# Kernel optimization log

Hardware: AMD Instinct MI355X
Metric: run time of the kernel (lower is better)

Reference implementation:

```python
import jax, jax.numpy as jnp
import numpy as np

HIDDEN = 2560
NUM_HEADS = 80
HEAD_DIM = 64
STATE = 128
N_GROUPS = 1
CONV_K = 4
CHUNK = 256
INTER = 2 * HIDDEN                       # 5120 = NUM_HEADS * HEAD_DIM
CONV_DIM = INTER + 2 * N_GROUPS * STATE  # 5376
PROJ = INTER + CONV_DIM + NUM_HEADS      # 10576
EPS = 1e-5
DT_MIN, DT_MAX = 0.0, 100.0


def segment_sum(x):
    # x: (..., T) -> (..., T, T); out[i, j] = sum_{j < k <= i} x[k], -inf above diag
    T = x.shape[-1]
    xe = jnp.broadcast_to(x[..., :, None], x.shape + (T,))  # [i, j] = x[i]
    mask_lo = jnp.tril(jnp.ones((T, T), dtype=bool), -1)
    seg = jnp.cumsum(jnp.where(mask_lo, xe, 0.0), axis=-2)
    mask = jnp.tril(jnp.ones((T, T), dtype=bool), 0)
    return jnp.where(mask, seg, -jnp.inf)


def setup_inputs() -> dict:
    key = jax.random.key(0)
    k0, k1, k2, k3 = jax.random.split(key, 4)
    x = jax.random.normal(k0, (2, 2048, HIDDEN), jnp.float32)
    in_proj_w = jax.random.normal(k1, (PROJ, HIDDEN), jnp.float32) * (HIDDEN ** -0.5)
    conv1d_w = jax.random.normal(k2, (CONV_DIM, CONV_K), jnp.float32) * (CONV_K ** -0.5)
    conv1d_b = jnp.zeros((CONV_DIM,), jnp.float32)
    A_log = jnp.log(jnp.arange(1, NUM_HEADS + 1, dtype=jnp.float32))
    D = jnp.ones((NUM_HEADS,), jnp.float32)
    dt_bias = jnp.ones((NUM_HEADS,), jnp.float32)
    norm_weight = jnp.ones((INTER,), jnp.float32)
    out_proj_w = jax.random.normal(k3, (HIDDEN, INTER), jnp.float32) * (INTER ** -0.5)
    return dict(input_states=x, in_proj_w=in_proj_w, conv1d_w=conv1d_w,
                conv1d_b=conv1d_b, A_log=A_log, D=D, dt_bias=dt_bias,
                norm_weight=norm_weight, out_proj_w=out_proj_w)


def _mamba2_forward(input_states, in_proj_w, conv1d_w, conv1d_b, A_log, D,
                    dt_bias, norm_weight, out_proj_w):
    b, s, _ = input_states.shape
    proj = input_states @ in_proj_w.T                       # (b, s, PROJ)
    gate, hs, dt = jnp.split(proj, [INTER, INTER + CONV_DIM], axis=-1)

    # causal depthwise conv1d + SiLU
    xT = jnp.transpose(hs, (0, 2, 1))                       # (b, conv_dim, s)
    xT = jnp.pad(xT, ((0, 0), (0, 0), (CONV_K - 1, 0)))
    conv = jax.lax.conv_general_dilated(
        xT, conv1d_w[:, None, :], (1,), 'VALID',
        feature_group_count=CONV_DIM, dimension_numbers=('NCH', 'OIH', 'NCH'))
    hs = jax.nn.silu(jnp.transpose(conv + conv1d_b[None, :, None], (0, 2, 1)))

    hs, B, C = jnp.split(hs, [INTER, INTER + N_GROUPS * STATE], axis=-1)
    A = -jnp.exp(A_log)                                     # (h,)
    dt = jnp.clip(jax.nn.softplus(dt + dt_bias), DT_MIN, DT_MAX)  # (b, s, h)

    X = hs.reshape(b, s, NUM_HEADS, HEAD_DIM)
    rep = NUM_HEADS // N_GROUPS
    B = jnp.repeat(B.reshape(b, s, N_GROUPS, STATE), rep, axis=2)
    C = jnp.repeat(C.reshape(b, s, N_GROUPS, STATE), rep, axis=2)

    pad = (-s) % CHUNK
    D_res = D[None, None, :, None] * jnp.pad(X, ((0, 0), (0, pad), (0, 0), (0, 0)))
    Xd = X * dt[..., None]                                  # discretized input
    dA = A[None, None, :] * dt                              # (b, s, h)

    def chunk(t):
        t = jnp.pad(t, [(0, 0), (0, pad)] + [(0, 0)] * (t.ndim - 2))
        return t.reshape(t.shape[0], -1, CHUNK, *t.shape[2:])

    Xc, Bc, Cc = chunk(Xd), chunk(B), chunk(C)              # (b, c, l, h, ...)
    Ac = jnp.transpose(chunk(dA), (0, 3, 1, 2))             # (b, h, c, l)
    A_cum = jnp.cumsum(Ac, axis=-1)

    # 1. intra-chunk (diagonal block) outputs
    L = jnp.exp(segment_sum(Ac))                            # (b, h, c, l, l)
    G = jnp.einsum('bclhn,bcshn->bhcls', Cc, Bc)
    Y_diag = jnp.einsum('bhcls,bcshp->bclhp', G * L, Xc)

    # 2. per-chunk final states
    decay_states = jnp.exp(A_cum[..., -1:] - A_cum)         # (b, h, c, l)
    states = jnp.einsum('bclhn,bhcl,bclhp->bchpn', Bc, decay_states, Xc)

    # 3. inter-chunk recurrence
    A_last = A_cum[..., -1]                                 # (b, h, c)
    decay_chunk = jnp.exp(segment_sum(jnp.pad(A_last, ((0, 0), (0, 0), (1, 0)))))
    states = jnp.concatenate([jnp.zeros_like(states[:, :1]), states], axis=1)
    new_states = jnp.einsum('bhzc,bchpn->bzhpn', decay_chunk, states)
    states = new_states[:, :-1]                             # (b, c, h, p, n)

    # 4. state -> output conversion
    Y_off = jnp.einsum('bclhn,bchpn,bhcl->bclhp', Cc, states, jnp.exp(A_cum))

    y = (Y_diag + Y_off).reshape(b, -1, NUM_HEADS, HEAD_DIM) + D_res
    y = y[:, :s].reshape(b, s, INTER)

    # gated RMSNorm
    y = y * jax.nn.silu(gate)
    var = jnp.mean(y * y, axis=-1, keepdims=True)
    y = y * jax.lax.rsqrt(var + EPS) * norm_weight
    return y @ out_proj_w.T


def reference(input_states, in_proj_w, conv1d_w, conv1d_b, A_log, D, dt_bias,
              norm_weight, out_proj_w):
    return _mamba2_forward(input_states, in_proj_w, conv1d_w, conv1d_b, A_log,
                           D, dt_bias, norm_weight, out_proj_w)
```

## Files before the change

kernel.cpp:

```cpp
#include <hip/hip_runtime.h>
#include <hip/hip_bf16.h>
#include <math.h>

#define HIDDEN   2560
#define NUM_HEADS 80
#define HEAD_DIM 64
#define STATE    128
#define CONV_K   4
#define CHUNK    256
#define INTER    (2*HIDDEN)
#define CONV_DIM (INTER + 2*STATE)
#define PROJ     (INTER + CONV_DIM + NUM_HEADS)
#define PROJ_PAD 10240
#define NBC      336
#define NBCP     384
#define EPS      1e-5f

#define BATCH 2
#define SEQ   2048
#define TOK   (BATCH*SEQ)
#define NC    (SEQ/CHUNK)
#define KSPL2 8
#define KCH2  (HIDDEN/KSPL2)

typedef __attribute__((ext_vector_type(8))) short bf16x8;
typedef __attribute__((ext_vector_type(4))) float f32x4;

#define MFMA16(a,b,c) __builtin_amdgcn_mfma_f32_16x16x32_bf16((a),(b),(c),0,0,0)

__device__ __forceinline__ unsigned short f2bf(float f){
    union{float f;unsigned u;}v; v.f=f;
    unsigned r = v.u + 0x7fffu + ((v.u>>16)&1u);
    return (unsigned short)(r>>16);
}
__device__ __forceinline__ float bf2f(unsigned short s){
    union{unsigned u;float f;}v; v.u = ((unsigned)s)<<16; return v.f;
}
__device__ __forceinline__ void unpack8(uint4 u, float* e){
    e[0]=bf2f((unsigned short)(u.x&0xffff)); e[1]=bf2f((unsigned short)(u.x>>16));
    e[2]=bf2f((unsigned short)(u.y&0xffff)); e[3]=bf2f((unsigned short)(u.y>>16));
    e[4]=bf2f((unsigned short)(u.z&0xffff)); e[5]=bf2f((unsigned short)(u.z>>16));
    e[6]=bf2f((unsigned short)(u.w&0xffff)); e[7]=bf2f((unsigned short)(u.w>>16));
}

__device__ __forceinline__ void gld16(const void* g, void* l){
    __builtin_amdgcn_global_load_lds((const __attribute__((address_space(1))) void*)g,
                                     (__attribute__((address_space(3))) void*)l, 16, 0, 0);
}

template<bool BF16OUT>
__global__ __launch_bounds__(256) void gemm_bf16(const unsigned short* __restrict__ A, int lda,
                                                 const unsigned short* __restrict__ B, int ldb,
                                                 void* __restrict__ Cv, int ldc, int K) {
    __shared__ unsigned short As[128][64];
    __shared__ unsigned short Bs[128][64];
    int tid = threadIdx.x;
    int lane = tid & 63, wid = tid >> 6;
    int wr = wid >> 1, wc = wid & 1;

    int bm, bn;
    if ((gridDim.y & 7) == 0) {
        int bid   = blockIdx.y * gridDim.x + blockIdx.x;
        int xcd   = bid & 7;
        int local = bid >> 3;
        int mrows = gridDim.y >> 3;
        bm = (xcd * mrows + (local % mrows)) * 128;
        bn = (local / mrows) * 128;
    } else {
        bm = blockIdx.y * 128;
        bn = blockIdx.x * 128;
    }

    f32x4 acc[4][4];
    #pragma unroll
    for (int i=0;i<4;i++)
        #pragma unroll
        for (int j=0;j<4;j++) acc[i][j] = (f32x4){0.f,0.f,0.f,0.f};

    int srow_off = lane >> 3;
    int sslot    = lane & 7;

    for (int k0 = 0; k0 < K; k0 += 64) {
        #pragma unroll
        for (int q=0;q<4;q++){
            int brow = (wid*4+q)*8;
            int row  = brow + srow_off;
            int sl   = sslot ^ (row & 7);
            gld16(A + (size_t)(bm + row)*lda + k0 + sl*8, &As[brow][0]);
            gld16(B + (size_t)(bn + row)*ldb + k0 + sl*8, &Bs[brow][0]);
        }
        __syncthreads();
        #pragma unroll
        for (int kk=0; kk<64; kk+=32){
            bf16x8 a[4], b[4];
            #pragma unroll
            for (int i=0;i<4;i++){
                int row = wr*64 + i*16 + (lane&15);
                int slot = ((kk>>3) + (lane>>4)) ^ (row & 7);
                a[i] = *(const bf16x8*)&As[row][slot*8];
            }
            #pragma unroll
            for (int j=0;j<4;j++){
                int row = wc*64 + j*16 + (lane&15);
                int slot = ((kk>>3) + (lane>>4)) ^ (row & 7);
                b[j] = *(const bf16x8*)&Bs[row][slot*8];
            }
            #pragma unroll
            for (int i=0;i<4;i++)
                #pragma unroll
                for (int j=0;j<4;j++)
                    acc[i][j] = MFMA16(a[i], b[j], acc[i][j]);
        }
        __syncthreads();
    }
    #pragma unroll
    for (int i=0;i<4;i++){
        int row0 = bm + wr*64 + i*16 + (lane>>4)*4;
        #pragma unroll
        for (int j=0;j<4;j++){
            int col = bn + wc*64 + j*16 + (lane&15);
            #pragma unroll
            for (int r=0;r<4;r++){
                if (BF16OUT)
                    ((unsigned short*)Cv)[(size_t)(row0+r)*ldc + col] = f2bf(acc[i][j][r]);
                else
                    ((float*)Cv)[(size_t)(row0+r)*ldc + col] = acc[i][j][r];
            }
        }
    }
}

__global__ __launch_bounds__(256) void bc_splitk_mfma(const unsigned short* __restrict__ xhi,
                                                      const unsigned short* __restrict__ xlo,
                                                      const unsigned short* __restrict__ whi,
                                                      const unsigned short* __restrict__ wlo,
                                                      float* __restrict__ Cpart) {
    __shared__ unsigned short As[128][64];
    __shared__ unsigned short Bs[128][64];
    int tid = threadIdx.x;
    int lane = tid & 63, wid = tid >> 6;
    int wr = wid >> 1, wc = wid & 1;
    int bn = blockIdx.x * 128, bm = blockIdx.y * 128, z = blockIdx.z;

    f32x4 acc[4][4];
    #pragma unroll
    for (int i=0;i<4;i++)
        #pragma unroll
        for (int j=0;j<4;j++) acc[i][j] = (f32x4){0.f,0.f,0.f,0.f};

    int srow_off = lane >> 3;
    int sslot    = lane & 7;

    for (int term = 0; term < 3; ++term){
        const unsigned short* A = (term==2) ? xlo : xhi;
        const unsigned short* B = (term==0) ? wlo : whi;
        for (int k0 = z*KCH2; k0 < z*KCH2 + KCH2; k0 += 64) {
            #pragma unroll
            for (int q=0;q<4;q++){
                int brow = (wid*4+q)*8;
                int row  = brow + srow_off;
                int sl   = sslot ^ (row & 7);
                gld16(A + (size_t)(bm + row)*HIDDEN + k0 + sl*8, &As[brow][0]);
                gld16(B + (size_t)(bn + row)*HIDDEN + k0 + sl*8, &Bs[brow][0]);
            }
            __syncthreads();
            #pragma unroll
            for (int kk=0; kk<64; kk+=32){
                bf16x8 a[4], b[4];
                #pragma unroll
                for (int i=0;i<4;i++){
                    int row = wr*64 + i*16 + (lane&15);
                    int slot = ((kk>>3) + (lane>>4)) ^ (row & 7);
                    a[i] = *(const bf16x8*)&As[row][slot*8];
                }
                #pragma unroll
                for (int j=0;j<4;j++){
                    int row = wc*64 + j*16 + (lane&15);
                    int slot = ((kk>>3) + (lane>>4)) ^ (row & 7);
                    b[j] = *(const bf16x8*)&Bs[row][slot*8];
                }
                #pragma unroll
                for (int i=0;i<4;i++)
                    #pragma unroll
                    for (int j=0;j<4;j++)
                        acc[i][j] = MFMA16(a[i], b[j], acc[i][j]);
            }
            __syncthreads();
        }
    }
    float* Cz = Cpart + (size_t)z*TOK*NBCP;
    #pragma unroll
    for (int i=0;i<4;i++){
        int row0 = bm + wr*64 + i*16 + (lane>>4)*4;
        #pragma unroll
        for (int j=0;j<4;j++){
            int col = bn + wc*64 + j*16 + (lane&15);
            #pragma unroll
            for (int r=0;r<4;r++)
                Cz[(size_t)(row0+r)*NBCP + col] = acc[i][j][r];
        }
    }
}

__global__ __launch_bounds__(256) void reduce_bc2(const float* __restrict__ part,
                                                  const float* __restrict__ dt_bias,
                                                  float* __restrict__ outBC,
                                                  float* __restrict__ dtbuf) {
    size_t i4 = (size_t)blockIdx.x*256 + threadIdx.x;
    if (i4 >= (size_t)TOK*NBCP/4) return;
    size_t i = i4*4;
    float4 s = *(const float4*)(part + i);
    #pragma unroll
    for (int z=1; z<KSPL2; z++){
        float4 v = *(const float4*)(part + (size_t)z*TOK*NBCP + i);
        s.x += v.x; s.y += v.y; s.z += v.z; s.w += v.w;
    }
    int col = (int)(i % NBCP);
    int t   = (int)(i / NBCP);
    if (col < 256) {
        *(float4*)(outBC + (size_t)t*NBC + col) = s;
    } else if (col < NBC) {
        int h = col - 256;
        float e[4] = {s.x, s.y, s.z, s.w};
        #pragma unroll
        for (int u=0;u<4;u++){
            float xv = e[u] + dt_bias[h+u];
            float sp = (xv > 20.f) ? xv : log1pf(expf(xv));
            e[u] = fminf(fmaxf(sp, 0.f), 100.f);
        }
        float4 o; o.x=e[0]; o.y=e[1]; o.z=e[2]; o.w=e[3];
        *(float4*)(dtbuf + (size_t)t*NUM_HEADS + h) = o;
    }
}

#define N4A ((size_t)TOK*HIDDEN/4)
#define N4B ((size_t)PROJ_PAD*HIDDEN/4)
#define N4C ((size_t)NBCP*HIDDEN/4)
__global__ __launch_bounds__(256) void prep_kernel(const float* __restrict__ x,
                                                   const float* __restrict__ in_w,
                                                   unsigned short* __restrict__ xhi,
                                                   unsigned short* __restrict__ xlo,
                                                   unsigned short* __restrict__ w1b,
                                                   unsigned short* __restrict__ wbc_hi,
                                                   unsigned short* __restrict__ wbc_lo) {
    size_t gid = (size_t)blockIdx.x*256 + threadIdx.x;
    if (gid < N4A) {
        size_t i = gid*4;
        float4 v = *(const float4*)(x + i);
        float e[4] = {v.x, v.y, v.z, v.w};
        ushort4 h, l;
        unsigned short* hp = (unsigned short*)&h;
        unsigned short* lp = (unsigned short*)&l;
        #pragma unroll
        for (int u=0;u<4;u++){
            unsigned short hv = f2bf(e[u]);
            hp[u] = hv;
            lp[u] = f2bf(e[u] - bf2f(hv));
        }
        *(ushort4*)(xhi + i) = h;
        *(ushort4*)(xlo + i) = l;
    } else if (gid < N4A + N4B) {
        size_t i = (gid - N4A)*4;
        float4 v = *(const float4*)(in_w + i);
        ushort4 o;
        o.x=f2bf(v.x); o.y=f2bf(v.y); o.z=f2bf(v.z); o.w=f2bf(v.w);
        *(ushort4*)(w1b + i) = o;
    } else {
        size_t j = gid - N4A - N4B;
        size_t i = j*4;
        int row = (int)(i / HIDDEN);
        int kk  = (int)(i % HIDDEN);
        ushort4 h, l;
        h.x=h.y=h.z=h.w=0; l.x=l.y=l.z=l.w=0;
        if (row < NBC){
            float4 v = *(const float4*)(in_w + (size_t)(2*INTER + row)*HIDDEN + kk);
            float e[4] = {v.x, v.y, v.z, v.w};
            unsigned short* hp = (unsigned short*)&h;
            unsigned short* lp = (unsigned short*)&l;
            #pragma unroll
            for (int u=0;u<4;u++){
                unsigned short hv = f2bf(e[u]);
                hp[u] = hv;
                lp[u] = f2bf(e[u] - bf2f(hv));
            }
        }
        *(ushort4*)(wbc_hi + i) = h;
        *(ushort4*)(wbc_lo + i) = l;
    }
}

__global__ __launch_bounds__(256) void cvt_bf16(const float* __restrict__ in,
                                                unsigned short* __restrict__ out, size_t n4){
    size_t i4 = (size_t)blockIdx.x*256 + threadIdx.x;
    if (i4 >= n4) return;
    size_t i = i4*4;
    float4 v = *(const float4*)(in+i);
    ushort4 o; o.x=f2bf(v.x); o.y=f2bf(v.y); o.z=f2bf(v.z); o.w=f2bf(v.w);
    *(ushort4*)(out+i) = o;
}

__global__ __launch_bounds__(256) void conv_fused(const unsigned short* __restrict__ projb,
                                                  const float* __restrict__ projBC,
                                                  const float* __restrict__ cw,
                                                  const float* __restrict__ cb,
                                                  unsigned short* __restrict__ XT,
                                                  float* __restrict__ xBC_BC,
                                                  unsigned short* __restrict__ BT,
                                                  unsigned short* __restrict__ Cb) {
    __shared__ unsigned short raw[68][66];
    int bid = blockIdx.x;
    int tid = threadIdx.x;
    if (bid < (TOK/64)*(INTER/64)) {
        int bx = bid & 63, by = bid >> 6;
        int t0 = bx * 64, d0 = by * 64;
        int b  = t0 / SEQ;
        int s0 = t0 % SEQ;
        for (int f = tid; f < 67*8; f += 256){
            int r = f >> 3, g = f & 7;
            int sp = s0 - 3 + r;
            uint4 v;
            if (sp >= 0) v = *(const uint4*)(projb + ((size_t)(b*SEQ+sp))*PROJ_PAD + INTER + d0 + g*8);
            else { v.x=0u; v.y=0u; v.z=0u; v.w=0u; }
            unsigned int* dst = (unsigned int*)&raw[r][g*8];
            dst[0]=v.x; dst[1]=v.y; dst[2]=v.z; dst[3]=v.w;
        }
        __syncthreads();
        int t = tid & 63, dg = tid >> 6;
        #pragma unroll
        for (int dd = 0; dd < 16; dd++){
            int d = dg*16 + dd;
            float acc = cb[d0+d];
            #pragma unroll
            for (int j=0;j<CONV_K;j++)
                acc += cw[(d0+d)*CONV_K+j] * bf2f(raw[t+j][d]);
            float val = acc/(1.f+expf(-acc));
            XT[((size_t)(b*INTER + d0 + d))*SEQ + s0 + t] = f2bf(val);
        }
    } else {
        int idx = (bid - (TOK/64)*(INTER/64))*256 + tid;
        if (idx >= TOK*256) return;
        int d = idx & 255;
        int t = idx >> 8;
        int b = t / SEQ, sl = t % SEQ;
        int dc = INTER + d;
        float acc = cb[dc];
        #pragma unroll
        for (int j=0;j<CONV_K;j++){
            int sp = sl - (CONV_K-1) + j;
            if (sp >= 0)
                acc += cw[dc*CONV_K+j] * projBC[((size_t)(b*SEQ+sp))*NBC + d];
        }
        float val = acc / (1.f + expf(-acc));
        xBC_BC[(size_t)t*256 + d] = val;
        if (d < 128)
            BT[((size_t)(b*128 + d))*SEQ + sl] = f2bf(val);
        else
            Cb[(size_t)t*128 + (d-128)] = f2bf(val);
    }
}

__global__ __launch_bounds__(256) void cumsum_kernel(const float* __restrict__ dtbuf,
                                                     const float* __restrict__ A_log,
                                                     float* __restrict__ A_cum) {
    int c = blockIdx.x, h = blockIdx.y, b = blockIdx.z;
    int l = threadIdx.x;
    float A = -expf(A_log[h]);
    float v = A * dtbuf[(size_t)(b*SEQ + c*CHUNK + l)*NUM_HEADS + h];
    __shared__ float buf[CHUNK];
    buf[l] = v;
    __syncthreads();
    for (int off=1; off<CHUNK; off<<=1){
        float t = (l>=off) ? buf[l-off] : 0.f;
        __syncthreads();
        buf[l] += t;
        __syncthreads();
    }
    A_cum[((size_t)b*NUM_HEADS + h)*SEQ + c*CHUNK + l] = buf[l];
}

__global__ __launch_bounds__(256) void g_kernel(const float* __restrict__ xBC_BC,
                                                unsigned short* __restrict__ G) {
    int p = blockIdx.x, c = blockIdx.y, b = blockIdx.z;
    int lt = 0, a0 = 0;
    while (a0 + lt + 1 <= p) { a0 += lt + 1; lt++; }
    int st = p - a0;
    int l0 = lt*64, s0 = st*64;
    __shared__ float Cs[64][68];
    __shared__ float Bs[64][68];
    int tid = threadIdx.x, ty = tid >> 4, tx = tid & 15;
    float acc[4][4];
    #pragma unroll
    for (int i=0;i<4;i++)
        #pragma unroll
        for (int j=0;j<4;j++) acc[i][j]=0.f;

    size_t rowC = ((size_t)(b*SEQ + c*CHUNK + l0))*256 + 128;
    size_t rowB = ((size_t)(b*SEQ + c*CHUNK + s0))*256;
    for (int kc=0; kc<2; kc++){
        #pragma unroll
        for (int it=0; it<4; it++){
            int f = tid + it*256;
            int r = f >> 4, c4 = f & 15;
            float4 cv = *(const float4*)(xBC_BC + rowC + (size_t)r*256 + kc*64 + c4*4);
            float4 bv = *(const float4*)(xBC_BC + rowB + (size_t)r*256 + kc*64 + c4*4);
            *(float4*)&Cs[r][c4*4] = cv;
            *(float4*)&Bs[r][c4*4] = bv;
        }
        __syncthreads();
        #pragma unroll 8
        for (int k=0;k<64;k++){
            float a[4], bb[4];
            #pragma unroll
            for (int i=0;i<4;i++) a[i] = Cs[ty*4+i][k];
            #pragma unroll
            for (int j=0;j<4;j++) bb[j] = Bs[tx*4+j][k];
            #pragma unroll
            for (int i=0;i<4;i++)
                #pragma unroll
                for (int j=0;j<4;j++) acc[i][j] += a[i]*bb[j];
        }
        __syncthreads();
    }
    size_t Gb = ((size_t)(b*NC + c)) << 16;
    #pragma unroll
    for (int i=0;i<4;i++){
        ushort4 g4;
        g4.x = f2bf(acc[i][0]); g4.y = f2bf(acc[i][1]);
        g4.z = f2bf(acc[i][2]); g4.w = f2bf(acc[i][3]);
        *(ushort4*)(G + Gb + (size_t)(l0 + ty*4 + i)*256 + s0 + tx*4) = g4;
    }
}

__global__ __launch_bounds__(256) void states_mfma(const unsigned short* __restrict__ XT,
                                                   const unsigned short* __restrict__ BT,
                                                   const float* __restrict__ dtbuf,
                                                   const float* __restrict__ A_cum,
                                                   unsigned short* __restrict__ statesT) {
    int c = blockIdx.x, h = blockIdx.y, b = blockIdx.z;
    __shared__ unsigned short Asx[64][64];
    __shared__ unsigned short Bs[128][64];
    __shared__ float wl[CHUNK];
    int tid = threadIdx.x, lane = tid & 63, wid = tid >> 6;
    {
        const float* ac = A_cum + ((size_t)(b*NUM_HEADS+h))*SEQ + c*CHUNK;
        float Alast = ac[CHUNK-1];
        wl[tid] = expf(Alast - ac[tid]) * dtbuf[((size_t)(b*SEQ + c*CHUNK + tid))*NUM_HEADS + h];
    }
    __syncthreads();
    f32x4 acc[4][2];
    #pragma unroll
    for (int i=0;i<4;i++)
        #pragma unroll
        for (int j=0;j<2;j++) acc[i][j] = (f32x4){0.f,0.f,0.f,0.f};

    for (int kc = 0; kc < 4; kc++){
        int lbase = kc*64;
        #pragma unroll
        for (int q=0;q<4;q++){
            int brow = (wid*4+q)*8;
            int row  = brow + (lane>>3);
            int sl   = (lane&7) ^ (row & 7);
            gld16(BT + ((size_t)(b*128 + row))*SEQ + c*CHUNK + lbase + sl*8, &Bs[brow][0]);
        }
        #pragma unroll
        for (int it=0; it<2; it++){
            int f = tid + it*256;
            int r = f >> 3, g = f & 7;
            uint4 v = *(const uint4*)(XT + ((size_t)(b*INTER + h*HEAD_DIM + r))*SEQ + c*CHUNK + lbase + g*8);
            float e[8]; unpack8(v, e);
            unsigned short o[8];
            #pragma unroll
            for (int u=0;u<8;u++) o[u] = f2bf(e[u] * wl[lbase + g*8 + u]);
            int slot = g ^ (r & 7);
            *(ushort4*)&Asx[r][slot*8]   = *(ushort4*)&o[0];
            *(ushort4*)&Asx[r][slot*8+4] = *(ushort4*)&o[4];
        }
        __syncthreads();
        #pragma unroll
        for (int kk=0; kk<64; kk+=32){
            bf16x8 a[4], bb[2];
            #pragma unroll
            for (int i=0;i<4;i++){
                int row = i*16 + (lane&15);
                int slot = ((kk>>3)+(lane>>4)) ^ (row&7);
                a[i] = *(const bf16x8*)&Asx[row][slot*8];
            }
            #pragma unroll
            for (int j=0;j<2;j++){
                int row = wid*32 + j*16 + (lane&15);
                int slot = ((kk>>3)+(lane>>4)) ^ (row&7);
                bb[j] = *(const bf16x8*)&Bs[row][slot*8];
            }
            #pragma unroll
            for (int i=0;i<4;i++)
                #pragma unroll
                for (int j=0;j<2;j++)
                    acc[i][j] = MFMA16(a[i], bb[j], acc[i][j]);
        }
        __syncthreads();
    }
    size_t sb = ((size_t)((b*NC + c)*NUM_HEADS + h))*(HEAD_DIM*STATE);
    #pragma unroll
    for (int i=0;i<4;i++){
        #pragma unroll
        for (int j=0;j<2;j++){
            int n = wid*32 + j*16 + (lane&15);
            int p0 = i*16 + (lane>>4)*4;
            #pragma unroll
            for (int r=0;r<4;r++)
                statesT[sb + (size_t)(p0+r)*128 + n] = f2bf(acc[i][j][r]);
        }
    }
}

__global__ __launch_bounds__(256) void recur_kernel(const float* __restrict__ A_cum,
                                                    unsigned short* __restrict__ states) {
    int h = blockIdx.x, b = blockIdx.y;
    int tid = threadIdx.x;
    float Srun[32];
    #pragma unroll
    for (int i=0;i<32;i++) Srun[i]=0.f;
    const float* acum = A_cum + ((size_t)b*NUM_HEADS + h)*SEQ;
    for (int c=0;c<NC;c++){
        float alast = acum[c*CHUNK + CHUNK-1];
        float dec = expf(alast);
        size_t base = ((size_t)((b*NC + c)*NUM_HEADS + h))*(HEAD_DIM*STATE);
        #pragma unroll
        for (int i=0;i<32;i++){
            size_t idx = base + (size_t)tid + (size_t)i*256;
            float raw = bf2f(states[idx]);
            states[idx] = f2bf(Srun[i]);
            Srun[i] = Srun[i]*dec + raw;
        }
    }
}

__global__ __launch_bounds__(256) void yscan_mfma(const unsigned short* __restrict__ G,
                                                  const unsigned short* __restrict__ Cb,
                                                  const unsigned short* __restrict__ XT,
                                                  const float* __restrict__ dtbuf,
                                                  const float* __restrict__ A_cum,
                                                  const unsigned short* __restrict__ statesT,
                                                  const float* __restrict__ Dvec,
                                                  unsigned short* __restrict__ projb) {
    int xb = blockIdx.x;
    int c = xb >> 2, lt = xb & 3;
    int h = blockIdx.y, b = blockIdx.z;
    int l0 = lt*64;
    __shared__ __align__(16) char pool[32768];
    unsigned short (*Cs)[128] = (unsigned short(*)[128])pool;
    unsigned short (*St)[128] = (unsigned short(*)[128])(pool + 16384);
    unsigned short (*Gw)[64]  = (unsigned short(*)[64])pool;
    unsigned short (*Xs)[64]  = (unsigned short(*)[64])(pool + 8192);
    float (*Ot)[68]           = (float(*)[68])pool;
    __shared__ float ac[CHUNK], dts[CHUNK];
    int tid = threadIdx.x, lane = tid & 63, wid = tid >> 6;
    ac[tid]  = A_cum[((size_t)(b*NUM_HEADS + h))*SEQ + c*CHUNK + tid];
    dts[tid] = dtbuf[((size_t)(b*SEQ + c*CHUNK + tid))*NUM_HEADS + h];

    size_t stb = ((size_t)((b*NC + c)*NUM_HEADS + h))*(HEAD_DIM*STATE);
    #pragma unroll
    for (int q=0;q<4;q++){
        int brow = (wid*4+q)*4;
        int row  = brow + (lane>>4);
        int sl   = (lane&15) ^ (row & 7);
        gld16(Cb + ((size_t)(b*SEQ + c*CHUNK + l0 + row))*128 + sl*8, &Cs[brow][0]);
        gld16(statesT + stb + (size_t)row*128 + sl*8, &St[brow][0]);
    }
    __syncthreads();

    f32x4 acc1[4];
    #pragma unroll
    for (int j=0;j<4;j++) acc1[j] = (f32x4){0.f,0.f,0.f,0.f};
    #pragma unroll
    for (int kk=0; kk<128; kk+=32){
        int arow = wid*16 + (lane&15);
        int aslot = ((kk>>3)+(lane>>4)) ^ (arow&7);
        bf16x8 a = *(const bf16x8*)&Cs[arow][aslot*8];
        #pragma unroll
        for (int j=0;j<4;j++){
            int brow = j*16 + (lane&15);
            int bslot = ((kk>>3)+(lane>>4)) ^ (brow&7);
            bf16x8 bb = *(const bf16x8*)&St[brow][bslot*8];
            acc1[j] = MFMA16(a, bb, acc1[j]);
        }
    }
    float el[4];
    #pragma unroll
    for (int r=0;r<4;r++) el[r] = expf(ac[l0 + wid*16 + (lane>>4)*4 + r]);
    float master[4][4];
    #pragma unroll
    for (int j=0;j<4;j++)
        #pragma unroll
        for (int r=0;r<4;r++) master[j][r] = acc1[j][r]*el[r];
    __syncthreads();

    size_t Gb = ((size_t)(b*NC + c)) << 16;
    f32x4 acc2[4];
    #pragma unroll
    for (int j=0;j<4;j++) acc2[j] = (f32x4){0.f,0.f,0.f,0.f};
    for (int st=0; st<=lt; st++){
        int s0 = st*64;
        #pragma unroll
        for (int it=0; it<2; it++){
            int f = tid + it*256;
            int r = f >> 3, g = f & 7;
            uint4 v = *(const uint4*)(G + Gb + (size_t)(l0 + r)*256 + s0 + g*8);
            float e[8]; unpack8(v, e);
            float acl = ac[l0 + r];
            unsigned short o[8];
            #pragma unroll
            for (int u=0;u<8;u++){
                int s = s0 + g*8 + u;
                float w = (s <= l0 + r) ? expf(acl - ac[s])*dts[s] : 0.f;
                o[u] = f2bf(e[u]*w);
            }
            int slot = g ^ (r&7);
            *(ushort4*)&Gw[r][slot*8]   = *(ushort4*)&o[0];
            *(ushort4*)&Gw[r][slot*8+4] = *(ushort4*)&o[4];
        }
        #pragma unroll
        for (int q=0;q<2;q++){
            int brow = (wid*2+q)*8;
            int row  = brow + (lane>>3);
            int sl   = (lane&7) ^ (row&7);
            gld16(XT + ((size_t)(b*INTER + h*HEAD_DIM + row))*SEQ + c*CHUNK + s0 + sl*8,
                  &Xs[brow][0]);
        }
        __syncthreads();
        #pragma unroll
        for (int kk=0; kk<64; kk+=32){
            int arow = wid*16 + (lane&15);
            int aslot = ((kk>>3)+(lane>>4)) ^ (arow&7);
            bf16x8 a = *(const bf16x8*)&Gw[arow][aslot*8];
            #pragma unroll
            for (int j=0;j<4;j++){
                int brow = j*16 + (lane&15);
                int bslot = ((kk>>3)+(lane>>4)) ^ (brow&7);
                bf16x8 bb = *(const bf16x8*)&Xs[brow][bslot*8];
                acc2[j] = MFMA16(a, bb, acc2[j]);
            }
        }
        if (st < lt) __syncthreads();
    }

    float Dh = Dvec[h];
    #pragma unroll
    for (int j=0;j<4;j++){
        int p = j*16 + (lane&15);
        #pragma unroll
        for (int r=0;r<4;r++){
            int sl_ = wid*16 + (lane>>4)*4 + r;
            int slot = (sl_>>3) ^ (p&7);
            float xv = bf2f(Xs[p][slot*8 + (sl_&7)]);
            master[j][r] += acc2[j][r] + Dh*xv;
        }
    }
    __syncthreads();

    #pragma unroll
    for (int j=0;j<4;j++){
        int p = j*16 + (lane&15);
        #pragma unroll
        for (int r=0;r<4;r++)
            Ot[wid*16 + (lane>>4)*4 + r][p] = master[j][r];
    }
    __syncthreads();
    #pragma unroll
    for (int it=0; it<4; it++){
        int f = tid + it*256;
        int r = f >> 4, c4 = f & 15;
        ushort4 o;
        o.x = f2bf(Ot[r][c4*4+0]); o.y = f2bf(Ot[r][c4*4+1]);
        o.z = f2bf(Ot[r][c4*4+2]); o.w = f2bf(Ot[r][c4*4+3]);
        *(ushort4*)(projb + ((size_t)(b*SEQ + c*CHUNK + l0 + r))*PROJ_PAD + INTER + h*HEAD_DIM + c4*4) = o;
    }
}

__global__ __launch_bounds__(256) void gate_norm_kernel(const unsigned short* __restrict__ projb,
                                                        const float* __restrict__ normw,
                                                        unsigned short* __restrict__ yb) {
    int t = blockIdx.x;
    int tid = threadIdx.x;
    const unsigned short* row = projb + (size_t)t*PROJ_PAD;
    __shared__ float red[4];
    float vals[20];
    float ss = 0.f;
    #pragma unroll
    for (int i=0;i<5;i++){
        int j = (tid + i*256)*4;
        ushort4 g4 = *(const ushort4*)(row + j);
        ushort4 y4 = *(const ushort4*)(row + INTER + j);
        #pragma unroll
        for (int u=0;u<4;u++){
            float g = bf2f(((const unsigned short*)&g4)[u]);
            float y = bf2f(((const unsigned short*)&y4)[u]);
            float gv = g / (1.f + expf(-g));
            float v = y * gv;
            vals[i*4+u] = v;
            ss += v*v;
        }
    }
    #pragma unroll
    for (int off=32; off; off>>=1) ss += __shfl_xor(ss, off);
    if ((tid&63)==0) red[tid>>6] = ss;
    __syncthreads();
    float tot = red[0]+red[1]+red[2]+red[3];
    float inv = rsqrtf(tot/(float)INTER + EPS);
    #pragma unroll
    for (int i=0;i<5;i++){
        int j = (tid + i*256)*4;
        ushort4 o;
        o.x = f2bf(vals[i*4+0] * inv * normw[j+0]);
        o.y = f2bf(vals[i*4+1] * inv * normw[j+1]);
        o.z = f2bf(vals[i*4+2] * inv * normw[j+2]);
        o.w = f2bf(vals[i*4+3] * inv * normw[j+3]);
        *(ushort4*)(yb + (size_t)t*INTER + j) = o;
    }
}

extern "C" void kernel_launch(void* const* d_in, const int* in_sizes, int n_in,
                              void* d_out, int out_size, void* d_ws, size_t ws_size,
                              hipStream_t stream) {
    const float* x        = (const float*)d_in[0];
    const float* in_w     = (const float*)d_in[1];
    const float* conv_w   = (const float*)d_in[2];
    const float* conv_b   = (const float*)d_in[3];
    const float* A_log    = (const float*)d_in[4];
    const float* Dvec     = (const float*)d_in[5];
    const float* dt_bias  = (const float*)d_in[6];
    const float* norm_w   = (const float*)d_in[7];
    const float* out_w    = (const float*)d_in[8];
    float* out = (float*)d_out;
    (void)ws_size; (void)n_in; (void)in_sizes; (void)out_size;

    const size_t PROJB   = (size_t)TOK*PROJ_PAD*2;
    const size_t PROJBCB = (size_t)TOK*NBC*4;
    const size_t XTB     = (size_t)TOK*INTER*2;
    const size_t XBCBCB  = (size_t)TOK*256*4;
    const size_t BTB     = (size_t)BATCH*128*SEQ*2;
    const size_t CBB     = (size_t)TOK*128*2;
    const size_t GBYTES  = (size_t)BATCH*NC*CHUNK*CHUNK*2;
    const size_t DTB     = (size_t)TOK*NUM_HEADS*4;
    const size_t ACUMB   = DTB;
    const size_t STB     = (size_t)BATCH*NC*NUM_HEADS*HEAD_DIM*STATE*2;
    const size_t XHB   = (size_t)TOK*HIDDEN*2;
    const size_t WBCB  = (size_t)NBCP*HIDDEN*2;
    const size_t YBB   = (size_t)TOK*INTER*2;

    char* base = (char*)d_ws;
    size_t off = 0;
    unsigned short* projb  = (unsigned short*)(base + off); off += PROJB;
    float* projBC          = (float*)(base + off);          off += PROJBCB;
    unsigned short* XTp    = (unsigned short*)(base + off); off += XTB;
    float* xBC_BC          = (float*)(base + off);          off += XBCBCB;
    unsigned short* BTp    = (unsigned short*)(base + off); off += BTB;
    unsigned short* Cbp    = (unsigned short*)(base + off); off += CBB;
    unsigned short* Gp     = (unsigned short*)(base + off); off += GBYTES;
    float* dtbuf           = (float*)(base + off);          off += DTB;
    float* A_cum           = (float*)(base + off);          off += ACUMB;
    unsigned short* statesT= (unsigned short*)(base + off); off += STB;
    char*  T               = base + off;
    unsigned short* xhi    = (unsigned short*)T;
    unsigned short* xlo    = (unsigned short*)(T + XHB);
    unsigned short* wbc_hi = (unsigned short*)(T + 2*XHB);
    unsigned short* wbc_lo = (unsigned short*)(T + 2*XHB + WBCB);
    unsigned short* w1b    = (unsigned short*)(T + 2*XHB + 2*WBCB);
    float* bcpart          = (float*)w1b;
    unsigned short* yb     = (unsigned short*)T;
    unsigned short* w2b    = (unsigned short*)(T + YBB);

    const size_t W2_E = (size_t)HIDDEN*INTER;

    {
        unsigned total_blocks = (unsigned)((N4A + N4B + N4C) / 256);
        prep_kernel<<<total_blocks, 256, 0, stream>>>(x, in_w, xhi, xlo, w1b, wbc_hi, wbc_lo);
    }
    gemm_bf16<true><<<dim3(PROJ_PAD/128, TOK/128), 256, 0, stream>>>(xhi, HIDDEN, w1b, HIDDEN,
                                                                     projb, PROJ_PAD, HIDDEN);
    bc_splitk_mfma<<<dim3(NBCP/128, TOK/128, KSPL2), 256, 0, stream>>>(xhi, xlo, wbc_hi, wbc_lo, bcpart);
    reduce_bc2<<<(unsigned)(((size_t)TOK*NBCP/4)/256), 256, 0, stream>>>(bcpart, dt_bias, projBC, dtbuf);
    conv_fused<<<(TOK/64)*(INTER/64) + TOK, 256, 0, stream>>>(projb, projBC, conv_w, conv_b,
                                                              XTp, xBC_BC, BTp, Cbp);
    cvt_bf16<<<(unsigned)((W2_E/4+255)/256), 256, 0, stream>>>(out_w, w2b, W2_E/4);
    cumsum_kernel<<<dim3(NC, NUM_HEADS, BATCH), 256, 0, stream>>>(dtbuf, A_log, A_cum);
    g_kernel<<<dim3(10, NC, BATCH), 256, 0, stream>>>(xBC_BC, Gp);
    states_mfma<<<dim3(NC, NUM_HEADS, BATCH), 256, 0, stream>>>(XTp, BTp, dtbuf, A_cum, statesT);
    recur_kernel<<<dim3(NUM_HEADS, BATCH), 256, 0, stream>>>(A_cum, statesT);
    yscan_mfma<<<dim3(NC*4, NUM_HEADS, BATCH), 256, 0, stream>>>(Gp, Cbp, XTp, dtbuf, A_cum,
                                                                 statesT, Dvec, projb);
    gate_norm_kernel<<<TOK, 256, 0, stream>>>(projb, norm_w, yb);
    gemm_bf16<false><<<dim3(HIDDEN/128, TOK/128), 256, 0, stream>>>(yb, INTER, w2b, INTER,
                                                                    out, HIDDEN, INTER);
}
```

Measured before the change: 726.8 us.

## Fuse weight conversion into conv kernel and split small kernels into more blocks

Folds the out_proj fp32-to-bf16 conversion into the conv_fused launch as extra blocks, removing one kernel launch. Retiles g_kernel to 32x32 tiles over the full K=128 in one shared-memory pass, giving 36 lower-triangle tiles per chunk instead of 10. Splits recur_kernel across 4 z-blocks so each holds 8 state registers instead of 32. Reorders yscan block indexing so consecutive blocks cover different chunks. The aim is more parallelism for latency-bound small kernels, at the cost of less per-thread register reuse in g_kernel.

Result: faster. 710.3 us (-2.3%).

```diff
diff --git a/kernel.cpp b/kernel.cpp
--- a/kernel.cpp
+++ b/kernel.cpp
@@ -289,28 +289,22 @@
     }
 }
 
-__global__ __launch_bounds__(256) void cvt_bf16(const float* __restrict__ in,
-                                                unsigned short* __restrict__ out, size_t n4){
-    size_t i4 = (size_t)blockIdx.x*256 + threadIdx.x;
-    if (i4 >= n4) return;
-    size_t i = i4*4;
-    float4 v = *(const float4*)(in+i);
-    ushort4 o; o.x=f2bf(v.x); o.y=f2bf(v.y); o.z=f2bf(v.z); o.w=f2bf(v.w);
-    *(ushort4*)(out+i) = o;
-}
-
+#define XBLK ((TOK/64)*(INTER/64))
+#define W2BLK ((int)(((size_t)HIDDEN*INTER/4)/256))
 __global__ __launch_bounds__(256) void conv_fused(const unsigned short* __restrict__ projb,
                                                   const float* __restrict__ projBC,
                                                   const float* __restrict__ cw,
                                                   const float* __restrict__ cb,
+                                                  const float* __restrict__ out_w,
                                                   unsigned short* __restrict__ XT,
                                                   float* __restrict__ xBC_BC,
                                                   unsigned short* __restrict__ BT,
-                                                  unsigned short* __restrict__ Cb) {
+                                                  unsigned short* __restrict__ Cb,
+                                                  unsigned short* __restrict__ w2b) {
     __shared__ unsigned short raw[68][66];
     int bid = blockIdx.x;
     int tid = threadIdx.x;
-    if (bid < (TOK/64)*(INTER/64)) {
+    if (bid < XBLK) {
         int bx = bid & 63, by = bid >> 6;
         int t0 = bx * 64, d0 = by * 64;
         int b  = t0 / SEQ;
@@ -336,9 +330,8 @@
             float val = acc/(1.f+expf(-acc));
             XT[((size_t)(b*INTER + d0 + d))*SEQ + s0 + t] = f2bf(val);
         }
-    } else {
-        int idx = (bid - (TOK/64)*(INTER/64))*256 + tid;
-        if (idx >= TOK*256) return;
+    } else if (bid < XBLK + TOK) {
+        int idx = (bid - XBLK)*256 + tid;
         int d = idx & 255;
         int t = idx >> 8;
         int b = t / SEQ, sl = t % SEQ;
@@ -356,6 +349,12 @@
             BT[((size_t)(b*128 + d))*SEQ + sl] = f2bf(val);
         else
             Cb[(size_t)t*128 + (d-128)] = f2bf(val);
+    } else {
+        size_t i4 = (size_t)(bid - XBLK - TOK)*256 + tid;
+        size_t i = i4*4;
+        float4 v = *(const float4*)(out_w + i);
+        ushort4 o; o.x=f2bf(v.x); o.y=f2bf(v.y); o.z=f2bf(v.z); o.w=f2bf(v.w);
+        *(ushort4*)(w2b + i) = o;
     }
 }
 
@@ -380,54 +379,40 @@
 
 __global__ __launch_bounds__(256) void g_kernel(const float* __restrict__ xBC_BC,
                                                 unsigned short* __restrict__ G) {
-    int p = blockIdx.x, c = blockIdx.y, b = blockIdx.z;
+    int c = blockIdx.x, p = blockIdx.y, b = blockIdx.z;
     int lt = 0, a0 = 0;
     while (a0 + lt + 1 <= p) { a0 += lt + 1; lt++; }
     int st = p - a0;
-    int l0 = lt*64, s0 = st*64;
-    __shared__ float Cs[64][68];
-    __shared__ float Bs[64][68];
+    int l0 = lt*32, s0 = st*32;
+    __shared__ float Cs[32][132];
+    __shared__ float Bs[32][132];
     int tid = threadIdx.x, ty = tid >> 4, tx = tid & 15;
-    float acc[4][4];
-    #pragma unroll
-    for (int i=0;i<4;i++)
-        #pragma unroll
-        for (int j=0;j<4;j++) acc[i][j]=0.f;
+    float acc[2][2];
+    acc[0][0]=0.f; acc[0][1]=0.f; acc[1][0]=0.f; acc[1][1]=0.f;
 
     size_t rowC = ((size_t)(b*SEQ + c*CHUNK + l0))*256 + 128;
     size_t rowB = ((size_t)(b*SEQ + c*CHUNK + s0))*256;
-    for (int kc=0; kc<2; kc++){
-        #pragma unroll
-        for (int it=0; it<4; it++){
-            int f = tid + it*256;
-            int r = f >> 4, c4 = f & 15;
-            float4 cv = *(const float4*)(xBC_BC + rowC + (size_t)r*256 + kc*64 + c4*4);
-            float4 bv = *(const float4*)(xBC_BC + rowB + (size_t)r*256 + kc*64 + c4*4);
-            *(float4*)&Cs[r][c4*4] = cv;
-            *(float4*)&Bs[r][c4*4] = bv;
-        }
-        __syncthreads();
-        #pragma unroll 8
-        for (int k=0;k<64;k++){
-            float a[4], bb[4];
-            #pragma unroll
-            for (int i=0;i<4;i++) a[i] = Cs[ty*4+i][k];
-            #pragma unroll
-            for (int j=0;j<4;j++) bb[j] = Bs[tx*4+j][k];
-            #pragma unroll
-            for (int i=0;i<4;i++)
-                #pragma unroll
-                for (int j=0;j<4;j++) acc[i][j] += a[i]*bb[j];
-        }
-        __syncthreads();
+    #pragma unroll
+    for (int it=0; it<4; it++){
+        int f = tid + it*256;
+        int r = f >> 5, c4 = f & 31;
+        *(float4*)&Cs[r][c4*4] = *(const float4*)(xBC_BC + rowC + (size_t)r*256 + c4*4);
+        *(float4*)&Bs[r][c4*4] = *(const float4*)(xBC_BC + rowB + (size_t)r*256 + c4*4);
+    }
+    __syncthreads();
+    #pragma unroll 8
+    for (int k=0;k<128;k++){
+        float a0v = Cs[ty*2][k],   a1v = Cs[ty*2+1][k];
+        float b0v = Bs[tx*2][k],   b1v = Bs[tx*2+1][k];
+        acc[0][0] += a0v*b0v; acc[0][1] += a0v*b1v;
+        acc[1][0] += a1v*b0v; acc[1][1] += a1v*b1v;
     }
     size_t Gb = ((size_t)(b*NC + c)) << 16;
     #pragma unroll
-    for (int i=0;i<4;i++){
-        ushort4 g4;
-        g4.x = f2bf(acc[i][0]); g4.y = f2bf(acc[i][1]);
-        g4.z = f2bf(acc[i][2]); g4.w = f2bf(acc[i][3]);
-        *(ushort4*)(G + Gb + (size_t)(l0 + ty*4 + i)*256 + s0 + tx*4) = g4;
+    for (int i=0;i<2;i++){
+        ushort2 g2;
+        g2.x = f2bf(acc[i][0]); g2.y = f2bf(acc[i][1]);
+        *(ushort2*)(G + Gb + (size_t)(l0 + ty*2 + i)*256 + s0 + tx*2) = g2;
     }
 }
 
@@ -515,19 +500,19 @@
 
 __global__ __launch_bounds__(256) void recur_kernel(const float* __restrict__ A_cum,
                                                     unsigned short* __restrict__ states) {
-    int h = blockIdx.x, b = blockIdx.y;
+    int h = blockIdx.x, b = blockIdx.y, z = blockIdx.z;
     int tid = threadIdx.x;
-    float Srun[32];
-    #pragma unroll
-    for (int i=0;i<32;i++) Srun[i]=0.f;
+    float Srun[8];
+    #pragma unroll
+    for (int i=0;i<8;i++) Srun[i]=0.f;
     const float* acum = A_cum + ((size_t)b*NUM_HEADS + h)*SEQ;
     for (int c=0;c<NC;c++){
         float alast = acum[c*CHUNK + CHUNK-1];
         float dec = expf(alast);
         size_t base = ((size_t)((b*NC + c)*NUM_HEADS + h))*(HEAD_DIM*STATE);
         #pragma unroll
-        for (int i=0;i<32;i++){
-            size_t idx = base + (size_t)tid + (size_t)i*256;
+        for (int i=0;i<8;i++){
+            size_t idx = base + (size_t)tid + (size_t)(z*8+i)*256;
             float raw = bf2f(states[idx]);
             states[idx] = f2bf(Srun[i]);
             Srun[i] = Srun[i]*dec + raw;
@@ -544,7 +529,7 @@
                                                   const float* __restrict__ Dvec,
                                                   unsigned short* __restrict__ projb) {
     int xb = blockIdx.x;
-    int c = xb >> 2, lt = xb & 3;
+    int c = xb & 7, lt = xb >> 3;
     int h = blockIdx.y, b = blockIdx.z;
     int l0 = lt*64;
     __shared__ __align__(16) char pool[32768];
@@ -770,8 +755,6 @@
     unsigned short* yb     = (unsigned short*)T;
     unsigned short* w2b    = (unsigned short*)(T + YBB);
 
-    const size_t W2_E = (size_t)HIDDEN*INTER;
-
     {
         unsigned total_blocks = (unsigned)((N4A + N4B + N4C) / 256);
         prep_kernel<<<total_blocks, 256, 0, stream>>>(x, in_w, xhi, xlo, w1b, wbc_hi, wbc_lo);
@@ -780,13 +763,12 @@
                                                                      projb, PROJ_PAD, HIDDEN);
     bc_splitk_mfma<<<dim3(NBCP/128, TOK/128, KSPL2), 256, 0, stream>>>(xhi, xlo, wbc_hi, wbc_lo, bcpart);
     reduce_bc2<<<(unsigned)(((size_t)TOK*NBCP/4)/256), 256, 0, stream>>>(bcpart, dt_bias, projBC, dtbuf);
-    conv_fused<<<(TOK/64)*(INTER/64) + TOK, 256, 0, stream>>>(projb, projBC, conv_w, conv_b,
-                                                              XTp, xBC_BC, BTp, Cbp);
-    cvt_bf16<<<(unsigned)((W2_E/4+255)/256), 256, 0, stream>>>(out_w, w2b, W2_E/4);
+    conv_fused<<<XBLK + TOK + W2BLK, 256, 0, stream>>>(projb, projBC, conv_w, conv_b, out_w,
+                                                       XTp, xBC_BC, BTp, Cbp, w2b);
     cumsum_kernel<<<dim3(NC, NUM_HEADS, BATCH), 256, 0, stream>>>(dtbuf, A_log, A_cum);
-    g_kernel<<<dim3(10, NC, BATCH), 256, 0, stream>>>(xBC_BC, Gp);
+    g_kernel<<<dim3(NC, 36, BATCH), 256, 0, stream>>>(xBC_BC, Gp);
     states_mfma<<<dim3(NC, NUM_HEADS, BATCH), 256, 0, stream>>>(XTp, BTp, dtbuf, A_cum, statesT);
-    recur_kernel<<<dim3(NUM_HEADS, BATCH), 256, 0, stream>>>(A_cum, statesT);
+    recur_kernel<<<dim3(NUM_HEADS, BATCH, 4), 256, 0, stream>>>(A_cum, statesT);
     yscan_mfma<<<dim3(NC*4, NUM_HEADS, BATCH), 256, 0, stream>>>(Gp, Cbp, XTp, dtbuf, A_cum,
                                                                  statesT, Dvec, projb);
     gate_norm_kernel<<<TOK, 256, 0, stream>>>(projb, norm_w, yb);
```
